# Kernel optimization log

Measured on AMD Instinct MI355X. Metric: run time of the kernel, lower is better.

## Reference

```python
import jax, jax.numpy as jnp
import numpy as np

EMBED_DIM = 528
NUM_HEADS = 8
HEAD_DIM = EMBED_DIM // NUM_HEADS  # 66


def setup_inputs() -> dict:
    key = jax.random.key(0)
    k1, k2, k3, k4, k5 = jax.random.split(key, 5)
    B, D, H, W, C = 1, 16, 16, 16, EMBED_DIM
    s = 1.0 / np.sqrt(C)
    return {
        "x": jax.random.normal(k1, (B, D, H, W, C), dtype=jnp.float32),
        "w_qkv": jax.random.uniform(k2, (3 * C, C), dtype=jnp.float32, minval=-s, maxval=s),
        "b_qkv": jax.random.uniform(k3, (3 * C,), dtype=jnp.float32, minval=-s, maxval=s),
        "w_proj": jax.random.uniform(k4, (C, C), dtype=jnp.float32, minval=-s, maxval=s),
        "b_proj": jax.random.uniform(k5, (C,), dtype=jnp.float32, minval=-s, maxval=s),
    }


def reference(x, w_qkv, b_qkv, w_proj, b_proj):
    B, D, H, W, C = x.shape
    N = D * H * W
    h, hd = NUM_HEADS, HEAD_DIM
    scaling = hd ** (-0.5)

    xt = x.reshape(B, N, C)
    # qkv projection: [B, N, 3C] -> [3, B, h, N, hd]
    qkv = xt @ w_qkv.T + b_qkv
    qkv = qkv.reshape(B, N, 3, h, hd).transpose(2, 0, 3, 1, 4)
    q, k, v = qkv[0], qkv[1], qkv[2]

    # full attention over all D*H*W tokens
    attn = jnp.einsum('bhqd,bhkd->bhqk', q, k) * scaling
    attn = jax.nn.softmax(attn, axis=-1)
    out = jnp.einsum('bhqk,bhkd->bhqd', attn, v)  # [B, h, N, hd]

    out = out.transpose(0, 2, 1, 3).reshape(B, N, h * hd)
    out = out @ w_proj.T + b_proj
    return out.reshape(B, D, H, W, C)
```

## Files before the change

kernel.cpp:

```cpp
#include <hip/hip_runtime.h>

typedef __attribute__((ext_vector_type(8))) short bf16x8;
typedef __attribute__((ext_vector_type(4))) float f32x4;
typedef __attribute__((ext_vector_type(16))) float f32x16;

#define DEV __device__ __forceinline__

static constexpr int N_TOK = 4096;
static constexpr int C     = 528;
static constexpr int NH    = 8;
static constexpr int HD    = 66;
static constexpr int HDP   = 96;
static constexpr int VD96  = 96;
static constexpr int KP    = 544;
static constexpr int NQKV  = 1584;
static constexpr int NQKVP = 1632;

DEV unsigned short f2bf(float f) {
    unsigned int u = __float_as_uint(f);
    u = (u + 0x7fffu + ((u >> 16) & 1u)) >> 16;
    return (unsigned short)u;
}
DEV float bf2f(unsigned short h) { return __uint_as_float(((unsigned int)h) << 16); }
DEV unsigned cvtpk2(float a, float b) {
    unsigned r;
    asm("v_cvt_pk_bf16_f32 %0, %1, %2" : "=v"(r) : "v"(a), "v"(b));
    return r;
}
DEV void plswap(unsigned &a, unsigned &b) {
    asm volatile("v_permlane32_swap_b32 %0, %1" : "+v"(a), "+v"(b));
}

__global__ void k_prep_x(const float* __restrict__ x, unsigned short* __restrict__ xb) {
    int idx = blockIdx.x * 256 + threadIdx.x;
    if (idx >= N_TOK * KP) return;
    int n = idx / KP, k = idx - n * KP;
    xb[idx] = (k < C) ? f2bf(x[n * C + k]) : (unsigned short)0;
}
__global__ void k_prep_wqkv(const float* __restrict__ w, unsigned short* __restrict__ wb) {
    int idx = blockIdx.x * 256 + threadIdx.x;
    if (idx >= NQKVP * KP) return;
    int n = idx / KP, k = idx - n * KP;
    wb[idx] = (n < NQKV && k < C) ? f2bf(w[n * C + k]) : (unsigned short)0;
}
__global__ void k_prep_wproj(const float* __restrict__ w, unsigned short* __restrict__ whi,
                             unsigned short* __restrict__ wlo) {
    int idx = blockIdx.x * 256 + threadIdx.x;
    if (idx >= KP * KP) return;
    int n = idx / KP, k = idx - n * KP;
    unsigned short hi = 0, lo = 0;
    if (n < C && k < C) {
        float v = w[n * C + k];
        hi = f2bf(v);
        lo = f2bf(v - bf2f(hi));
    }
    whi[idx] = hi; wlo[idx] = lo;
}
__global__ void k_zero_pads(unsigned short* __restrict__ ahi, unsigned short* __restrict__ alo) {
    int idx = blockIdx.x * 256 + threadIdx.x;
    if (idx >= N_TOK * (KP - C)) return;
    int n = idx >> 4, c = C + (idx & 15);
    ahi[n * KP + c] = 0; alo[n * KP + c] = 0;
}

__launch_bounds__(256)
__global__ void k_gemm_qkv(const unsigned short* __restrict__ A,
                           const unsigned short* __restrict__ B,
                           const float* __restrict__ bias,
                           unsigned short* __restrict__ Cout) {
    constexpr int BM = 128, BN = 96, LDA = 40, LDB = 40;
    __shared__ unsigned short Al[BM * LDA];
    __shared__ unsigned short Bl[BN * LDB];
    int tid = threadIdx.x, lane = tid & 63, wid = tid >> 6;
    int m0 = blockIdx.x * BM, n0 = blockIdx.y * BN;
    int wm = (wid >> 1) * 64;
    int wn = (wid & 1) * 48;
    f32x4 acc[4][3] = {};
    for (int k0 = 0; k0 < KP; k0 += 32) {
        __syncthreads();
#pragma unroll
        for (int i = 0; i < 2; i++) {
            int c = i * 256 + tid;
            int row = c >> 2, kc = (c & 3) * 8;
            *(bf16x8*)&Al[row * LDA + kc] = *(const bf16x8*)&A[(m0 + row) * KP + k0 + kc];
        }
        {
            int c = tid, row = c >> 2, kc = (c & 3) * 8;
            *(bf16x8*)&Bl[row * LDB + kc] = *(const bf16x8*)&B[(n0 + row) * KP + k0 + kc];
            c = 256 + tid;
            if (c < 384) {
                row = c >> 2; kc = (c & 3) * 8;
                *(bf16x8*)&Bl[row * LDB + kc] = *(const bf16x8*)&B[(n0 + row) * KP + k0 + kc];
            }
        }
        __syncthreads();
        int kk = (lane >> 4) * 8;
        bf16x8 af[4], bfr[3];
#pragma unroll
        for (int mi = 0; mi < 4; mi++) af[mi] = *(const bf16x8*)&Al[(wm + mi * 16 + (lane & 15)) * LDA + kk];
#pragma unroll
        for (int ni = 0; ni < 3; ni++) bfr[ni] = *(const bf16x8*)&Bl[(wn + ni * 16 + (lane & 15)) * LDB + kk];
#pragma unroll
        for (int mi = 0; mi < 4; mi++)
#pragma unroll
            for (int ni = 0; ni < 3; ni++)
                acc[mi][ni] = __builtin_amdgcn_mfma_f32_16x16x32_bf16(af[mi], bfr[ni], acc[mi][ni], 0, 0, 0);
    }
#pragma unroll
    for (int mi = 0; mi < 4; mi++)
#pragma unroll
        for (int ni = 0; ni < 3; ni++)
#pragma unroll
            for (int r = 0; r < 4; r++) {
                int row = m0 + wm + mi * 16 + (lane >> 4) * 4 + r;
                int col = n0 + wn + ni * 16 + (lane & 15);
                float v = acc[mi][ni][r] + (col < NQKV ? bias[col] : 0.f);
                Cout[row * NQKVP + col] = f2bf(v);
            }
}

__global__ void k_scatter_qk(const unsigned short* __restrict__ T,
                             unsigned short* __restrict__ qb, unsigned short* __restrict__ kb) {
    int idx = blockIdx.x * 256 + threadIdx.x;
    if (idx >= NH * N_TOK * HDP) return;
    int d = idx % HDP;
    int n = (idx / HDP) & (N_TOK - 1);
    int h = idx / (HDP * N_TOK);
    unsigned short zq = 0, zk = 0;
    if (d < HD) {
        zq = T[n * NQKVP + h * HD + d];
        zk = T[n * NQKVP + C + h * HD + d];
    }
    qb[idx] = zq; kb[idx] = zk;
}

__global__ void k_transpose_v(const unsigned short* __restrict__ T, unsigned short* __restrict__ vt) {
    __shared__ unsigned short lt[64 * 104];
    int h = blockIdx.y, n0 = blockIdx.x * 64, tid = threadIdx.x;
#pragma unroll
    for (int i = 0; i < 24; i++) {
        int idx = i * 256 + tid;
        int ni = idx / 96, d = idx - ni * 96;
        unsigned short v = 0;
        if (d < HD) v = T[(n0 + ni) * NQKVP + 2 * C + h * HD + d];
        lt[ni * 104 + d] = v;
    }
    __syncthreads();
#pragma unroll
    for (int i = 0; i < 24; i++) {
        int idx = i * 256 + tid;
        int d = idx >> 6, ni = idx & 63;
        vt[((size_t)h * VD96 + d) * N_TOK + n0 + ni] = lt[ni * 104 + d];
    }
}

__launch_bounds__(512, 2)
__global__ void k_attn(const unsigned short* __restrict__ qb,
                       const unsigned short* __restrict__ kb,
                       const unsigned short* __restrict__ vt,
                       unsigned short* __restrict__ ahi,
                       unsigned short* __restrict__ alo) {
    __shared__ __align__(16) unsigned short Kl[2][128 * 128];
    __shared__ __align__(16) unsigned short Vl[2][96 * 128];
    int tid = threadIdx.x, lane = tid & 63, wid = tid >> 6;
    int wq = wid & 3, kh = wid >> 2;
    int hi = lane >> 5, lq = lane & 31;
    int bid = blockIdx.x;
    int head = bid & 7;
    int q0 = (bid >> 3) * 128;
    const float SC2 = 0.12309149097933274f * 1.4426950408889634f;

    bf16x8 aq[6];
    {
        const unsigned short* qrow = qb + ((size_t)head * N_TOK + q0 + wq * 32 + lq) * HDP + hi * 8;
#pragma unroll
        for (int t = 0; t < 6; t++) aq[t] = *(const bf16x8*)&qrow[t * 16];
    }
    f32x16 o0 = {}, o1 = {}, o2 = {};
    float m_r = -3e38f, l_r = 0.f;

    const unsigned short* kg = kb + (size_t)head * N_TOK * HDP;
    const unsigned short* vg = vt + (size_t)head * VD96 * N_TOK;

#pragma unroll
    for (int i = 0; i < 3; i++) {
        int c = i * 512 + tid;
        int row = c / 12, ch = c - row * 12;
        *(bf16x8*)&Kl[0][row * 128 + ((ch ^ (row & 15)) << 3)] =
            *(const bf16x8*)&kg[(size_t)row * HDP + ch * 8];
    }
#pragma unroll
    for (int i = 0; i < 3; i++) {
        int c = i * 512 + tid;
        int row = c >> 4, ch = c & 15;
        *(bf16x8*)&Vl[0][row * 128 + ((ch ^ (row & 15)) << 3)] =
            *(const bf16x8*)&vg[(size_t)row * N_TOK + ch * 8];
    }
    __syncthreads();

    for (int kt = 0; kt < 32; kt++) {
        int cur = kt & 1;
        bf16x8 gk[3], gv[3];
        if (kt < 31) {
            int n1 = (kt + 1) * 128;
#pragma unroll
            for (int i = 0; i < 3; i++) {
                int c = i * 512 + tid;
                int row = c / 12, ch = c - row * 12;
                gk[i] = *(const bf16x8*)&kg[(size_t)(n1 + row) * HDP + ch * 8];
            }
#pragma unroll
            for (int i = 0; i < 3; i++) {
                int c = i * 512 + tid;
                int row = c >> 4, ch = c & 15;
                gv[i] = *(const bf16x8*)&vg[(size_t)row * N_TOK + n1 + ch * 8];
            }
        }

        f32x16 s0 = {}, s1 = {};
        {
            int r0 = kh * 64 + lq, r1 = r0 + 32;
#pragma unroll
            for (int t = 0; t < 6; t++) {
                bf16x8 ka0 = *(const bf16x8*)&Kl[cur][r0 * 128 + (((2 * t + hi) ^ (r0 & 15)) << 3)];
                bf16x8 ka1 = *(const bf16x8*)&Kl[cur][r1 * 128 + (((2 * t + hi) ^ (r1 & 15)) << 3)];
                s0 = __builtin_amdgcn_mfma_f32_32x32x16_bf16(ka0, aq[t], s0, 0, 0, 0);
                s1 = __builtin_amdgcn_mfma_f32_32x32x16_bf16(ka1, aq[t], s1, 0, 0, 0);
            }
        }

        float mx = s0[0];
#pragma unroll
        for (int r = 1; r < 16; r++) mx = fmaxf(mx, s0[r]);
#pragma unroll
        for (int r = 0; r < 16; r++) mx = fmaxf(mx, s1[r]);
        mx = fmaxf(mx, __shfl_xor(mx, 32, 64));
        float mnew = fmaxf(m_r, mx);
        float fct = __builtin_amdgcn_exp2f((m_r - mnew) * SC2);
        m_r = mnew;
        float nb = mnew * SC2;
        float lsum = 0.f;
#pragma unroll
        for (int r = 0; r < 16; r++) { s0[r] = __builtin_amdgcn_exp2f(__builtin_fmaf(s0[r], SC2, -nb)); lsum += s0[r]; }
#pragma unroll
        for (int r = 0; r < 16; r++) { s1[r] = __builtin_amdgcn_exp2f(__builtin_fmaf(s1[r], SC2, -nb)); lsum += s1[r]; }
        lsum += __shfl_xor(lsum, 32, 64);
        l_r = l_r * fct + lsum;
#pragma unroll
        for (int r = 0; r < 16; r++) { o0[r] *= fct; o1[r] *= fct; o2[r] *= fct; }

        unsigned u0[2][4], u1[2][4];
#pragma unroll
        for (int a = 0; a < 4; a++) {
            u0[0][a] = cvtpk2(s0[4 * a + 0], s0[4 * a + 1]);
            u1[0][a] = cvtpk2(s0[4 * a + 2], s0[4 * a + 3]);
            u0[1][a] = cvtpk2(s1[4 * a + 0], s1[4 * a + 1]);
            u1[1][a] = cvtpk2(s1[4 * a + 2], s1[4 * a + 3]);
        }
#pragma unroll
        for (int kb2 = 0; kb2 < 2; kb2++)
#pragma unroll
            for (int a0 = 0; a0 < 4; a0 += 2) {
                plswap(u0[kb2][a0], u0[kb2][a0 + 1]);
                plswap(u1[kb2][a0], u1[kb2][a0 + 1]);
            }

#pragma unroll
        for (int t2 = 0; t2 < 4; t2++) {
            int kb2 = t2 >> 1, a0 = (t2 & 1) * 2;
            union { unsigned u[4]; bf16x8 v; } pf;
            pf.u[0] = u0[kb2][a0];     pf.u[1] = u1[kb2][a0];
            pf.u[2] = u0[kb2][a0 + 1]; pf.u[3] = u1[kb2][a0 + 1];
            int ch = kh * 8 + 2 * t2 + hi;
            int rv0 = lq, rv1 = 32 + lq, rv2 = 64 + lq;
            bf16x8 va0 = *(const bf16x8*)&Vl[cur][rv0 * 128 + ((ch ^ (rv0 & 15)) << 3)];
            bf16x8 va1 = *(const bf16x8*)&Vl[cur][rv1 * 128 + ((ch ^ (rv1 & 15)) << 3)];
            bf16x8 va2 = *(const bf16x8*)&Vl[cur][rv2 * 128 + ((ch ^ (rv2 & 15)) << 3)];
            o0 = __builtin_amdgcn_mfma_f32_32x32x16_bf16(va0, pf.v, o0, 0, 0, 0);
            o1 = __builtin_amdgcn_mfma_f32_32x32x16_bf16(va1, pf.v, o1, 0, 0, 0);
            o2 = __builtin_amdgcn_mfma_f32_32x32x16_bf16(va2, pf.v, o2, 0, 0, 0);
        }

        if (kt < 31) {
            int nxt = cur ^ 1;
#pragma unroll
            for (int i = 0; i < 3; i++) {
                int c = i * 512 + tid;
                int row = c / 12, ch = c - row * 12;
                *(bf16x8*)&Kl[nxt][row * 128 + ((ch ^ (row & 15)) << 3)] = gk[i];
            }
#pragma unroll
            for (int i = 0; i < 3; i++) {
                int c = i * 512 + tid;
                int row = c >> 4, ch = c & 15;
                *(bf16x8*)&Vl[nxt][row * 128 + ((ch ^ (row & 15)) << 3)] = gv[i];
            }
        }
        __syncthreads();
    }

    float* xc = (float*)&Kl[0][0];
    float* rg = xc + (size_t)(wq * 64 + lane) * 52;
    if (kh == 1) {
#pragma unroll
        for (int r = 0; r < 16; r++) rg[r] = o0[r];
#pragma unroll
        for (int r = 0; r < 16; r++) rg[16 + r] = o1[r];
#pragma unroll
        for (int r = 0; r < 16; r++) rg[32 + r] = o2[r];
        rg[48] = m_r; rg[49] = l_r;
    }
    __syncthreads();
    if (kh == 0) {
        float m1 = rg[48], l1 = rg[49];
        float m12 = fmaxf(m_r, m1);
        float f0 = __builtin_amdgcn_exp2f((m_r - m12) * SC2);
        float f1 = __builtin_amdgcn_exp2f((m1 - m12) * SC2);
        float inv = 1.f / (l_r * f0 + l1 * f1);
        int token = q0 + wq * 32 + lq;
#pragma unroll
        for (int db = 0; db < 3; db++) {
#pragma unroll
            for (int r = 0; r < 16; r++) {
                int d = db * 32 + (r & 3) + 8 * (r >> 2) + 4 * hi;
                if (d < HD) {
                    float own = (db == 0) ? o0[r] : (db == 1) ? o1[r] : o2[r];
                    float val = (own * f0 + rg[db * 16 + r] * f1) * inv;
                    unsigned short hb = f2bf(val);
                    float lo = val - bf2f(hb);
                    size_t a = (size_t)token * KP + head * HD + d;
                    ahi[a] = hb; alo[a] = f2bf(lo);
                }
            }
        }
    }
}

__launch_bounds__(256)
__global__ void k_gemm_proj(const unsigned short* __restrict__ Ahi_, const unsigned short* __restrict__ Alo_,
                            const unsigned short* __restrict__ Whi_, const unsigned short* __restrict__ Wlo_,
                            const float* __restrict__ bias, float* __restrict__ out) {
    constexpr int BM = 128, BN = 32, LDA = 40, LDB = 40;
    __shared__ unsigned short Ah[BM * LDA], Alw[BM * LDA], Bh[BN * LDB], Blw[BN * LDB];
    int tid = threadIdx.x, lane = tid & 63, wid = tid >> 6;
    int m0 = blockIdx.x * BM, n0 = blockIdx.y * BN;
    int wm = wid * 32;
    f32x4 acc[2][2] = {};
    for (int k0 = 0; k0 < KP; k0 += 32) {
        __syncthreads();
#pragma unroll
        for (int i = 0; i < 2; i++) {
            int c = i * 256 + tid;
            int row = c >> 2, kc = (c & 3) * 8;
            *(bf16x8*)&Ah[row * LDA + kc]  = *(const bf16x8*)&Ahi_[(size_t)(m0 + row) * KP + k0 + kc];
            *(bf16x8*)&Alw[row * LDA + kc] = *(const bf16x8*)&Alo_[(size_t)(m0 + row) * KP + k0 + kc];
        }
        if (tid < 128) {
            int row = tid >> 2, kc = (tid & 3) * 8;
            *(bf16x8*)&Bh[row * LDB + kc]  = *(const bf16x8*)&Whi_[(size_t)(n0 + row) * KP + k0 + kc];
            *(bf16x8*)&Blw[row * LDB + kc] = *(const bf16x8*)&Wlo_[(size_t)(n0 + row) * KP + k0 + kc];
        }
        __syncthreads();
        int kk = (lane >> 4) * 8;
        bf16x8 ah[2], al[2], bh[2], bl[2];
#pragma unroll
        for (int mi = 0; mi < 2; mi++) {
            ah[mi] = *(const bf16x8*)&Ah[(wm + mi * 16 + (lane & 15)) * LDA + kk];
            al[mi] = *(const bf16x8*)&Alw[(wm + mi * 16 + (lane & 15)) * LDA + kk];
        }
#pragma unroll
        for (int ni = 0; ni < 2; ni++) {
            bh[ni] = *(const bf16x8*)&Bh[(ni * 16 + (lane & 15)) * LDB + kk];
            bl[ni] = *(const bf16x8*)&Blw[(ni * 16 + (lane & 15)) * LDB + kk];
        }
#pragma unroll
        for (int mi = 0; mi < 2; mi++)
#pragma unroll
            for (int ni = 0; ni < 2; ni++) {
                acc[mi][ni] = __builtin_amdgcn_mfma_f32_16x16x32_bf16(ah[mi], bh[ni], acc[mi][ni], 0, 0, 0);
                acc[mi][ni] = __builtin_amdgcn_mfma_f32_16x16x32_bf16(ah[mi], bl[ni], acc[mi][ni], 0, 0, 0);
                acc[mi][ni] = __builtin_amdgcn_mfma_f32_16x16x32_bf16(al[mi], bh[ni], acc[mi][ni], 0, 0, 0);
            }
    }
#pragma unroll
    for (int mi = 0; mi < 2; mi++)
#pragma unroll
        for (int ni = 0; ni < 2; ni++)
#pragma unroll
            for (int r = 0; r < 4; r++) {
                int row = m0 + wm + mi * 16 + (lane >> 4) * 4 + r;
                int col = n0 + ni * 16 + (lane & 15);
                if (col < C) out[(size_t)row * C + col] = acc[mi][ni][r] + bias[col];
            }
}

extern "C" void kernel_launch(void* const* d_in, const int* in_sizes, int n_in,
                              void* d_out, int out_size, void* d_ws, size_t ws_size,
                              hipStream_t stream) {
    const float* x      = (const float*)d_in[0];
    const float* w_qkv  = (const float*)d_in[1];
    const float* b_qkv  = (const float*)d_in[2];
    const float* w_proj = (const float*)d_in[3];
    const float* b_proj = (const float*)d_in[4];
    float* out = (float*)d_out;
    char* ws = (char*)d_ws;

    const size_t o_xb     = 0;
    const size_t o_wqkvb  = o_xb     + 4456448;
    const size_t o_whi    = o_wqkvb  + 1775616;
    const size_t o_wlo    = o_whi    + 591872;
    const size_t o_qkvtmp = o_wlo    + 591872;
    const size_t o_qbf    = o_qkvtmp + 13369344;
    const size_t o_kbf    = o_qbf    + 6291456;
    const size_t o_vt     = o_kbf    + 6291456;
    const size_t need     = o_vt + 6291456;
    if (ws_size < need) return;

    unsigned short* xb     = (unsigned short*)(ws + o_xb);
    unsigned short* wqkvb  = (unsigned short*)(ws + o_wqkvb);
    unsigned short* whi    = (unsigned short*)(ws + o_whi);
    unsigned short* wlo    = (unsigned short*)(ws + o_wlo);
    unsigned short* qkvtmp = (unsigned short*)(ws + o_qkvtmp);
    unsigned short* qbf    = (unsigned short*)(ws + o_qbf);
    unsigned short* kbf    = (unsigned short*)(ws + o_kbf);
    unsigned short* vt     = (unsigned short*)(ws + o_vt);
    unsigned short* ahi    = xb;
    unsigned short* alo    = qkvtmp;

    k_prep_x    <<<(N_TOK * KP + 255) / 256, 256, 0, stream>>>(x, xb);
    k_prep_wqkv <<<(NQKVP * KP + 255) / 256, 256, 0, stream>>>(w_qkv, wqkvb);
    k_prep_wproj<<<(KP * KP + 255) / 256, 256, 0, stream>>>(w_proj, whi, wlo);
    k_gemm_qkv  <<<dim3(N_TOK / 128, NQKVP / 96), 256, 0, stream>>>(xb, wqkvb, b_qkv, qkvtmp);
    k_scatter_qk<<<(NH * N_TOK * HDP + 255) / 256, 256, 0, stream>>>(qkvtmp, qbf, kbf);
    k_transpose_v<<<dim3(N_TOK / 64, NH), 256, 0, stream>>>(qkvtmp, vt);
    k_zero_pads <<<(N_TOK * (KP - C) + 255) / 256, 256, 0, stream>>>(ahi, alo);
    k_attn      <<<dim3(256), 512, 0, stream>>>(qbf, kbf, vt, ahi, alo);
    k_gemm_proj <<<dim3(N_TOK / 128, KP / 32), 256, 0, stream>>>(ahi, alo, whi, wlo, b_proj, out);
}
```

Measured before the change: 147.3 us.

## Fuse prep and reshape kernels, double-buffer GEMMs, lazily rescale softmax

Three prep kernels become one grid-stride kernel, and the Q/K scatter and V transpose become one kernel using a z grid dimension. The pad-zeroing kernel is dropped, which relies on the zero pad columns of the weights cancelling any pad contents. Both GEMMs now double-buffer LDS with a register prefetch of the next K tile, and the projection GEMM widens its N tile to 64. The attention kernel rescales its running max and accumulators only when some lane's max grows past a threshold, which removes per-tile rescale multiplies at some risk to numerics.

```diff
diff --git a/kernel.cpp b/kernel.cpp
--- a/kernel.cpp
+++ b/kernel.cpp
@@ -31,36 +31,33 @@
     asm volatile("v_permlane32_swap_b32 %0, %1" : "+v"(a), "+v"(b));
 }
 
-__global__ void k_prep_x(const float* __restrict__ x, unsigned short* __restrict__ xb) {
-    int idx = blockIdx.x * 256 + threadIdx.x;
-    if (idx >= N_TOK * KP) return;
-    int n = idx / KP, k = idx - n * KP;
-    xb[idx] = (k < C) ? f2bf(x[n * C + k]) : (unsigned short)0;
-}
-__global__ void k_prep_wqkv(const float* __restrict__ w, unsigned short* __restrict__ wb) {
-    int idx = blockIdx.x * 256 + threadIdx.x;
-    if (idx >= NQKVP * KP) return;
-    int n = idx / KP, k = idx - n * KP;
-    wb[idx] = (n < NQKV && k < C) ? f2bf(w[n * C + k]) : (unsigned short)0;
-}
-__global__ void k_prep_wproj(const float* __restrict__ w, unsigned short* __restrict__ whi,
-                             unsigned short* __restrict__ wlo) {
-    int idx = blockIdx.x * 256 + threadIdx.x;
-    if (idx >= KP * KP) return;
-    int n = idx / KP, k = idx - n * KP;
-    unsigned short hi = 0, lo = 0;
-    if (n < C && k < C) {
-        float v = w[n * C + k];
-        hi = f2bf(v);
-        lo = f2bf(v - bf2f(hi));
-    }
-    whi[idx] = hi; wlo[idx] = lo;
-}
-__global__ void k_zero_pads(unsigned short* __restrict__ ahi, unsigned short* __restrict__ alo) {
-    int idx = blockIdx.x * 256 + threadIdx.x;
-    if (idx >= N_TOK * (KP - C)) return;
-    int n = idx >> 4, c = C + (idx & 15);
-    ahi[n * KP + c] = 0; alo[n * KP + c] = 0;
+__global__ void k_prep_all(const float* __restrict__ x, const float* __restrict__ w_qkv,
+                           const float* __restrict__ w_proj,
+                           unsigned short* __restrict__ xb, unsigned short* __restrict__ wqkvb,
+                           unsigned short* __restrict__ whi, unsigned short* __restrict__ wlo) {
+    const int T0 = N_TOK * KP;
+    const int T1 = T0 + NQKVP * KP;
+    const int T2 = T1 + KP * KP;
+    for (int idx = blockIdx.x * 256 + threadIdx.x; idx < T2; idx += gridDim.x * 256) {
+        if (idx < T0) {
+            int n = idx / KP, k = idx - n * KP;
+            xb[idx] = (k < C) ? f2bf(x[n * C + k]) : (unsigned short)0;
+        } else if (idx < T1) {
+            int j = idx - T0;
+            int n = j / KP, k = j - n * KP;
+            wqkvb[j] = (n < NQKV && k < C) ? f2bf(w_qkv[n * C + k]) : (unsigned short)0;
+        } else {
+            int j = idx - T1;
+            int n = j / KP, k = j - n * KP;
+            unsigned short hi = 0, lo = 0;
+            if (n < C && k < C) {
+                float v = w_proj[n * C + k];
+                hi = f2bf(v);
+                lo = f2bf(v - bf2f(hi));
+            }
+            whi[j] = hi; wlo[j] = lo;
+        }
+    }
 }
 
 __launch_bounds__(256)
@@ -68,43 +65,56 @@
                            const unsigned short* __restrict__ B,
                            const float* __restrict__ bias,
                            unsigned short* __restrict__ Cout) {
-    constexpr int BM = 128, BN = 96, LDA = 40, LDB = 40;
-    __shared__ unsigned short Al[BM * LDA];
-    __shared__ unsigned short Bl[BN * LDB];
+    constexpr int LDA = 40;
+    __shared__ unsigned short Al[2][128 * LDA];
+    __shared__ unsigned short Bl[2][96 * LDA];
     int tid = threadIdx.x, lane = tid & 63, wid = tid >> 6;
-    int m0 = blockIdx.x * BM, n0 = blockIdx.y * BN;
-    int wm = (wid >> 1) * 64;
-    int wn = (wid & 1) * 48;
+    int m0 = blockIdx.x * 128, n0 = blockIdx.y * 96;
+    int wm = (wid >> 1) * 64, wn = (wid & 1) * 48;
+    int arow0 = tid >> 2, arow1 = (256 + tid) >> 2, akc = (tid & 3) * 8;
+    bool bhave = tid < 128;
+    int brow1 = (256 + tid) >> 2;
     f32x4 acc[4][3] = {};
-    for (int k0 = 0; k0 < KP; k0 += 32) {
-        __syncthreads();
-#pragma unroll
-        for (int i = 0; i < 2; i++) {
-            int c = i * 256 + tid;
-            int row = c >> 2, kc = (c & 3) * 8;
-            *(bf16x8*)&Al[row * LDA + kc] = *(const bf16x8*)&A[(m0 + row) * KP + k0 + kc];
-        }
-        {
-            int c = tid, row = c >> 2, kc = (c & 3) * 8;
-            *(bf16x8*)&Bl[row * LDB + kc] = *(const bf16x8*)&B[(n0 + row) * KP + k0 + kc];
-            c = 256 + tid;
-            if (c < 384) {
-                row = c >> 2; kc = (c & 3) * 8;
-                *(bf16x8*)&Bl[row * LDB + kc] = *(const bf16x8*)&B[(n0 + row) * KP + k0 + kc];
-            }
-        }
-        __syncthreads();
-        int kk = (lane >> 4) * 8;
+    bf16x8 ra0, ra1, rb0, rb1;
+
+    ra0 = *(const bf16x8*)&A[(size_t)(m0 + arow0) * KP + akc];
+    ra1 = *(const bf16x8*)&A[(size_t)(m0 + arow1) * KP + akc];
+    rb0 = *(const bf16x8*)&B[(size_t)(n0 + arow0) * KP + akc];
+    if (bhave) rb1 = *(const bf16x8*)&B[(size_t)(n0 + brow1) * KP + akc];
+    *(bf16x8*)&Al[0][arow0 * LDA + akc] = ra0;
+    *(bf16x8*)&Al[0][arow1 * LDA + akc] = ra1;
+    *(bf16x8*)&Bl[0][arow0 * LDA + akc] = rb0;
+    if (bhave) *(bf16x8*)&Bl[0][brow1 * LDA + akc] = rb1;
+    __syncthreads();
+
+    int kk = (lane >> 4) * 8, cc = lane & 15;
+    for (int kt = 0; kt < 17; kt++) {
+        int cur = kt & 1;
+        if (kt < 16) {
+            int k0 = (kt + 1) * 32;
+            ra0 = *(const bf16x8*)&A[(size_t)(m0 + arow0) * KP + k0 + akc];
+            ra1 = *(const bf16x8*)&A[(size_t)(m0 + arow1) * KP + k0 + akc];
+            rb0 = *(const bf16x8*)&B[(size_t)(n0 + arow0) * KP + k0 + akc];
+            if (bhave) rb1 = *(const bf16x8*)&B[(size_t)(n0 + brow1) * KP + k0 + akc];
+        }
         bf16x8 af[4], bfr[3];
 #pragma unroll
-        for (int mi = 0; mi < 4; mi++) af[mi] = *(const bf16x8*)&Al[(wm + mi * 16 + (lane & 15)) * LDA + kk];
-#pragma unroll
-        for (int ni = 0; ni < 3; ni++) bfr[ni] = *(const bf16x8*)&Bl[(wn + ni * 16 + (lane & 15)) * LDB + kk];
+        for (int mi = 0; mi < 4; mi++) af[mi] = *(const bf16x8*)&Al[cur][(wm + mi * 16 + cc) * LDA + kk];
+#pragma unroll
+        for (int ni = 0; ni < 3; ni++) bfr[ni] = *(const bf16x8*)&Bl[cur][(wn + ni * 16 + cc) * LDA + kk];
 #pragma unroll
         for (int mi = 0; mi < 4; mi++)
 #pragma unroll
             for (int ni = 0; ni < 3; ni++)
                 acc[mi][ni] = __builtin_amdgcn_mfma_f32_16x16x32_bf16(af[mi], bfr[ni], acc[mi][ni], 0, 0, 0);
+        if (kt < 16) {
+            int nxt = cur ^ 1;
+            *(bf16x8*)&Al[nxt][arow0 * LDA + akc] = ra0;
+            *(bf16x8*)&Al[nxt][arow1 * LDA + akc] = ra1;
+            *(bf16x8*)&Bl[nxt][arow0 * LDA + akc] = rb0;
+            if (bhave) *(bf16x8*)&Bl[nxt][brow1 * LDA + akc] = rb1;
+        }
+        __syncthreads();
     }
 #pragma unroll
     for (int mi = 0; mi < 4; mi++)
@@ -113,44 +123,46 @@
 #pragma unroll
             for (int r = 0; r < 4; r++) {
                 int row = m0 + wm + mi * 16 + (lane >> 4) * 4 + r;
-                int col = n0 + wn + ni * 16 + (lane & 15);
+                int col = n0 + wn + ni * 16 + cc;
                 float v = acc[mi][ni][r] + (col < NQKV ? bias[col] : 0.f);
-                Cout[row * NQKVP + col] = f2bf(v);
-            }
-}
-
-__global__ void k_scatter_qk(const unsigned short* __restrict__ T,
-                             unsigned short* __restrict__ qb, unsigned short* __restrict__ kb) {
-    int idx = blockIdx.x * 256 + threadIdx.x;
-    if (idx >= NH * N_TOK * HDP) return;
-    int d = idx % HDP;
-    int n = (idx / HDP) & (N_TOK - 1);
-    int h = idx / (HDP * N_TOK);
-    unsigned short zq = 0, zk = 0;
-    if (d < HD) {
-        zq = T[n * NQKVP + h * HD + d];
-        zk = T[n * NQKVP + C + h * HD + d];
-    }
-    qb[idx] = zq; kb[idx] = zk;
-}
-
-__global__ void k_transpose_v(const unsigned short* __restrict__ T, unsigned short* __restrict__ vt) {
-    __shared__ unsigned short lt[64 * 104];
+                Cout[(size_t)row * NQKVP + col] = f2bf(v);
+            }
+}
+
+__global__ void k_reshape(const unsigned short* __restrict__ T,
+                          unsigned short* __restrict__ qb, unsigned short* __restrict__ kbuf,
+                          unsigned short* __restrict__ vt) {
     int h = blockIdx.y, n0 = blockIdx.x * 64, tid = threadIdx.x;
-#pragma unroll
-    for (int i = 0; i < 24; i++) {
-        int idx = i * 256 + tid;
-        int ni = idx / 96, d = idx - ni * 96;
-        unsigned short v = 0;
-        if (d < HD) v = T[(n0 + ni) * NQKVP + 2 * C + h * HD + d];
-        lt[ni * 104 + d] = v;
-    }
-    __syncthreads();
-#pragma unroll
-    for (int i = 0; i < 24; i++) {
-        int idx = i * 256 + tid;
-        int d = idx >> 6, ni = idx & 63;
-        vt[((size_t)h * VD96 + d) * N_TOK + n0 + ni] = lt[ni * 104 + d];
+    if (blockIdx.z == 0) {
+#pragma unroll
+        for (int i = 0; i < 24; i++) {
+            int idx = i * 256 + tid;
+            int ni = idx / 96, d = idx - ni * 96;
+            unsigned short zq = 0, zk = 0;
+            if (d < HD) {
+                zq = T[(size_t)(n0 + ni) * NQKVP + h * HD + d];
+                zk = T[(size_t)(n0 + ni) * NQKVP + C + h * HD + d];
+            }
+            size_t a = ((size_t)h * N_TOK + n0 + ni) * HDP + d;
+            qb[a] = zq; kbuf[a] = zk;
+        }
+    } else {
+        __shared__ unsigned short lt[64 * 104];
+#pragma unroll
+        for (int i = 0; i < 24; i++) {
+            int idx = i * 256 + tid;
+            int ni = idx / 96, d = idx - ni * 96;
+            unsigned short v = 0;
+            if (d < HD) v = T[(size_t)(n0 + ni) * NQKVP + 2 * C + h * HD + d];
+            lt[ni * 104 + d] = v;
+        }
+        __syncthreads();
+#pragma unroll
+        for (int i = 0; i < 24; i++) {
+            int idx = i * 256 + tid;
+            int d = idx >> 6, ni = idx & 63;
+            vt[((size_t)h * VD96 + d) * N_TOK + n0 + ni] = lt[ni * 104 + d];
+        }
     }
 }
 
@@ -235,19 +247,22 @@
 #pragma unroll
         for (int r = 0; r < 16; r++) mx = fmaxf(mx, s1[r]);
         mx = fmaxf(mx, __shfl_xor(mx, 32, 64));
-        float mnew = fmaxf(m_r, mx);
-        float fct = __builtin_amdgcn_exp2f((m_r - mnew) * SC2);
-        m_r = mnew;
-        float nb = mnew * SC2;
+        if (!__all((mx - m_r) * SC2 <= 8.f)) {
+            float mnew = fmaxf(m_r, mx);
+            float fct = __builtin_amdgcn_exp2f((m_r - mnew) * SC2);
+            m_r = mnew;
+            l_r *= fct;
+#pragma unroll
+            for (int r = 0; r < 16; r++) { o0[r] *= fct; o1[r] *= fct; o2[r] *= fct; }
+        }
+        float nb = m_r * SC2;
         float lsum = 0.f;
 #pragma unroll
         for (int r = 0; r < 16; r++) { s0[r] = __builtin_amdgcn_exp2f(__builtin_fmaf(s0[r], SC2, -nb)); lsum += s0[r]; }
 #pragma unroll
         for (int r = 0; r < 16; r++) { s1[r] = __builtin_amdgcn_exp2f(__builtin_fmaf(s1[r], SC2, -nb)); lsum += s1[r]; }
         lsum += __shfl_xor(lsum, 32, 64);
-        l_r = l_r * fct + lsum;
-#pragma unroll
-        for (int r = 0; r < 16; r++) { o0[r] *= fct; o1[r] *= fct; o2[r] *= fct; }
+        l_r += lsum;
 
         unsigned u0[2][4], u1[2][4];
 #pragma unroll
@@ -340,56 +355,82 @@
 __global__ void k_gemm_proj(const unsigned short* __restrict__ Ahi_, const unsigned short* __restrict__ Alo_,
                             const unsigned short* __restrict__ Whi_, const unsigned short* __restrict__ Wlo_,
                             const float* __restrict__ bias, float* __restrict__ out) {
-    constexpr int BM = 128, BN = 32, LDA = 40, LDB = 40;
-    __shared__ unsigned short Ah[BM * LDA], Alw[BM * LDA], Bh[BN * LDB], Blw[BN * LDB];
+    constexpr int LDA = 40;
+    __shared__ unsigned short Ah[2][128 * LDA], Aw[2][128 * LDA];
+    __shared__ unsigned short Bh[2][64 * LDA],  Bw[2][64 * LDA];
     int tid = threadIdx.x, lane = tid & 63, wid = tid >> 6;
-    int m0 = blockIdx.x * BM, n0 = blockIdx.y * BN;
+    int m0 = blockIdx.x * 128, n0 = blockIdx.y * 64;
     int wm = wid * 32;
-    f32x4 acc[2][2] = {};
-    for (int k0 = 0; k0 < KP; k0 += 32) {
-        __syncthreads();
-#pragma unroll
-        for (int i = 0; i < 2; i++) {
-            int c = i * 256 + tid;
-            int row = c >> 2, kc = (c & 3) * 8;
-            *(bf16x8*)&Ah[row * LDA + kc]  = *(const bf16x8*)&Ahi_[(size_t)(m0 + row) * KP + k0 + kc];
-            *(bf16x8*)&Alw[row * LDA + kc] = *(const bf16x8*)&Alo_[(size_t)(m0 + row) * KP + k0 + kc];
-        }
-        if (tid < 128) {
-            int row = tid >> 2, kc = (tid & 3) * 8;
-            *(bf16x8*)&Bh[row * LDB + kc]  = *(const bf16x8*)&Whi_[(size_t)(n0 + row) * KP + k0 + kc];
-            *(bf16x8*)&Blw[row * LDB + kc] = *(const bf16x8*)&Wlo_[(size_t)(n0 + row) * KP + k0 + kc];
-        }
-        __syncthreads();
-        int kk = (lane >> 4) * 8;
-        bf16x8 ah[2], al[2], bh[2], bl[2];
+    int arow0 = tid >> 2, arow1 = (256 + tid) >> 2, akc = (tid & 3) * 8;
+    bool bok = (n0 + arow0) < KP;
+    f32x4 acc[2][4] = {};
+    bf16x8 rah0, rah1, ral0, ral1, rbh, rbl;
+    const bf16x8 zero8 = {};
+
+    rah0 = *(const bf16x8*)&Ahi_[(size_t)(m0 + arow0) * KP + akc];
+    rah1 = *(const bf16x8*)&Ahi_[(size_t)(m0 + arow1) * KP + akc];
+    ral0 = *(const bf16x8*)&Alo_[(size_t)(m0 + arow0) * KP + akc];
+    ral1 = *(const bf16x8*)&Alo_[(size_t)(m0 + arow1) * KP + akc];
+    rbh = bok ? *(const bf16x8*)&Whi_[(size_t)(n0 + arow0) * KP + akc] : zero8;
+    rbl = bok ? *(const bf16x8*)&Wlo_[(size_t)(n0 + arow0) * KP + akc] : zero8;
+    *(bf16x8*)&Ah[0][arow0 * LDA + akc] = rah0;
+    *(bf16x8*)&Ah[0][arow1 * LDA + akc] = rah1;
+    *(bf16x8*)&Aw[0][arow0 * LDA + akc] = ral0;
+    *(bf16x8*)&Aw[0][arow1 * LDA + akc] = ral1;
+    *(bf16x8*)&Bh[0][arow0 * LDA + akc] = rbh;
+    *(bf16x8*)&Bw[0][arow0 * LDA + akc] = rbl;
+    __syncthreads();
+
+    int kk = (lane >> 4) * 8, cc = lane & 15;
+    for (int kt = 0; kt < 17; kt++) {
+        int cur = kt & 1;
+        if (kt < 16) {
+            int k0 = (kt + 1) * 32;
+            rah0 = *(const bf16x8*)&Ahi_[(size_t)(m0 + arow0) * KP + k0 + akc];
+            rah1 = *(const bf16x8*)&Ahi_[(size_t)(m0 + arow1) * KP + k0 + akc];
+            ral0 = *(const bf16x8*)&Alo_[(size_t)(m0 + arow0) * KP + k0 + akc];
+            ral1 = *(const bf16x8*)&Alo_[(size_t)(m0 + arow1) * KP + k0 + akc];
+            rbh = bok ? *(const bf16x8*)&Whi_[(size_t)(n0 + arow0) * KP + k0 + akc] : zero8;
+            rbl = bok ? *(const bf16x8*)&Wlo_[(size_t)(n0 + arow0) * KP + k0 + akc] : zero8;
+        }
+        bf16x8 ah[2], al[2], bh[4], bl[4];
 #pragma unroll
         for (int mi = 0; mi < 2; mi++) {
-            ah[mi] = *(const bf16x8*)&Ah[(wm + mi * 16 + (lane & 15)) * LDA + kk];
-            al[mi] = *(const bf16x8*)&Alw[(wm + mi * 16 + (lane & 15)) * LDA + kk];
-        }
-#pragma unroll
-        for (int ni = 0; ni < 2; ni++) {
-            bh[ni] = *(const bf16x8*)&Bh[(ni * 16 + (lane & 15)) * LDB + kk];
-            bl[ni] = *(const bf16x8*)&Blw[(ni * 16 + (lane & 15)) * LDB + kk];
+            ah[mi] = *(const bf16x8*)&Ah[cur][(wm + mi * 16 + cc) * LDA + kk];
+            al[mi] = *(const bf16x8*)&Aw[cur][(wm + mi * 16 + cc) * LDA + kk];
+        }
+#pragma unroll
+        for (int ni = 0; ni < 4; ni++) {
+            bh[ni] = *(const bf16x8*)&Bh[cur][(ni * 16 + cc) * LDA + kk];
+            bl[ni] = *(const bf16x8*)&Bw[cur][(ni * 16 + cc) * LDA + kk];
         }
 #pragma unroll
         for (int mi = 0; mi < 2; mi++)
 #pragma unroll
-            for (int ni = 0; ni < 2; ni++) {
+            for (int ni = 0; ni < 4; ni++) {
                 acc[mi][ni] = __builtin_amdgcn_mfma_f32_16x16x32_bf16(ah[mi], bh[ni], acc[mi][ni], 0, 0, 0);
                 acc[mi][ni] = __builtin_amdgcn_mfma_f32_16x16x32_bf16(ah[mi], bl[ni], acc[mi][ni], 0, 0, 0);
                 acc[mi][ni] = __builtin_amdgcn_mfma_f32_16x16x32_bf16(al[mi], bh[ni], acc[mi][ni], 0, 0, 0);
             }
+        if (kt < 16) {
+            int nxt = cur ^ 1;
+            *(bf16x8*)&Ah[nxt][arow0 * LDA + akc] = rah0;
+            *(bf16x8*)&Ah[nxt][arow1 * LDA + akc] = rah1;
+            *(bf16x8*)&Aw[nxt][arow0 * LDA + akc] = ral0;
+            *(bf16x8*)&Aw[nxt][arow1 * LDA + akc] = ral1;
+            *(bf16x8*)&Bh[nxt][arow0 * LDA + akc] = rbh;
+            *(bf16x8*)&Bw[nxt][arow0 * LDA + akc] = rbl;
+        }
+        __syncthreads();
     }
 #pragma unroll
     for (int mi = 0; mi < 2; mi++)
 #pragma unroll
-        for (int ni = 0; ni < 2; ni++)
+        for (int ni = 0; ni < 4; ni++)
 #pragma unroll
             for (int r = 0; r < 4; r++) {
                 int row = m0 + wm + mi * 16 + (lane >> 4) * 4 + r;
-                int col = n0 + ni * 16 + (lane & 15);
+                int col = n0 + ni * 16 + cc;
                 if (col < C) out[(size_t)row * C + col] = acc[mi][ni][r] + bias[col];
             }
 }
@@ -427,13 +468,9 @@
     unsigned short* ahi    = xb;
     unsigned short* alo    = qkvtmp;
 
-    k_prep_x    <<<(N_TOK * KP + 255) / 256, 256, 0, stream>>>(x, xb);
-    k_prep_wqkv <<<(NQKVP * KP + 255) / 256, 256, 0, stream>>>(w_qkv, wqkvb);
-    k_prep_wproj<<<(KP * KP + 255) / 256, 256, 0, stream>>>(w_proj, whi, wlo);
+    k_prep_all  <<<2048, 256, 0, stream>>>(x, w_qkv, w_proj, xb, wqkvb, whi, wlo);
     k_gemm_qkv  <<<dim3(N_TOK / 128, NQKVP / 96), 256, 0, stream>>>(xb, wqkvb, b_qkv, qkvtmp);
-    k_scatter_qk<<<(NH * N_TOK * HDP + 255) / 256, 256, 0, stream>>>(qkvtmp, qbf, kbf);
-    k_transpose_v<<<dim3(N_TOK / 64, NH), 256, 0, stream>>>(qkvtmp, vt);
-    k_zero_pads <<<(N_TOK * (KP - C) + 255) / 256, 256, 0, stream>>>(ahi, alo);
+    k_reshape   <<<dim3(N_TOK / 64, NH, 2), 256, 0, stream>>>(qkvtmp, qbf, kbf, vt);
     k_attn      <<<dim3(256), 512, 0, stream>>>(qbf, kbf, vt, ahi, alo);
-    k_gemm_proj <<<dim3(N_TOK / 128, KP / 32), 256, 0, stream>>>(ahi, alo, whi, wlo, b_proj, out);
-}
+    k_gemm_proj <<<dim3(N_TOK / 128, 9), 256, 0, stream>>>(ahi, alo, whi, wlo, b_proj, out);
+}
```

Measured after the change: 124.1 us. 15.7% less time.
